# Kernel tuning notes

Measured on AMD Instinct MI355X. Metric: run time of the kernel, lower is better.

The kernel has to match this reference:

```python
import jax, jax.numpy as jnp
import numpy as np

MIN_STD = 0.1
MAX_STD = 1.0
LOG2PI = float(np.log(2.0 * np.pi))


def setup_inputs() -> dict:
    key = jax.random.key(0)
    ks = jax.random.split(key, 5)
    B, D, N, L, H = 512, 256, 32768, 128, 512
    x = jax.random.normal(ks[0], (B, D), dtype=jnp.float32)
    log_w = jax.random.normal(ks[1], (N,), dtype=jnp.float32)
    z = jax.random.normal(ks[2], (N, L), dtype=jnp.float32)
    W1 = jax.random.normal(ks[3], (L, H), dtype=jnp.float32) * (1.0 / np.sqrt(L))
    b1 = jnp.zeros((H,), dtype=jnp.float32)
    W2 = jax.random.normal(ks[4], (H, 2 * D), dtype=jnp.float32) * (1.0 / np.sqrt(H))
    b2 = jnp.zeros((2 * D,), dtype=jnp.float32)
    return {"x": x, "log_w": log_w, "z": z, "W1": W1, "b1": b1, "W2": W2, "b2": b2, "k": 16}


def _get_params(zz, W1, b1, W2, b2):
    # net: 2-layer MLP, then chunk into (mu, logvar); std = clamp(softplus(logvar)+min_std)
    h = jax.nn.relu(zz @ W1 + b1)
    raw = h @ W2 + b2
    mu, logvar = jnp.split(raw, 2, axis=1)
    std = jnp.clip(jax.nn.softplus(logvar) + MIN_STD, MIN_STD, MAX_STD)
    return mu, std


def reference(x, log_w, z, W1, b1, W2, b2, k):
    B, D = x.shape
    # ---- stage 1 (torch.no_grad): full [B, N] Gaussian log-likelihood matrix ----
    mu, std = _get_params(z, W1, b1, W2, b2)          # [N, D]
    inv_var = 1.0 / (std * std)                        # [N, D]
    # sum_d logN(x_d; mu_d, std_d) expanded into matmuls to avoid a [B,N,D] tensor
    lp = (-0.5 * (x * x) @ inv_var.T                   # [B, N]
          + x @ (mu * inv_var).T
          - 0.5 * jnp.sum(mu * mu * inv_var, axis=1)[None, :]
          - jnp.sum(jnp.log(std), axis=1)[None, :]
          - 0.5 * D * LOG2PI)
    scores = lp + log_w[None, :]                       # [B, N]
    _, idx = jax.lax.top_k(scores, k)                  # [B, k]
    z_top = z[idx]                                     # [B, k, L] gather
    # ---- stage 2: recompute NLL only for the top-k components (with grad) ----
    mu2, std2 = _get_params(z_top.reshape(B * k, -1), W1, b1, W2, b2)
    mu2 = mu2.reshape(B, k, D)
    std2 = std2.reshape(B, k, D)
    diff = (x[:, None, :] - mu2) / std2                # [B, k, D]
    lp_topk = jnp.sum(-0.5 * diff * diff - jnp.log(std2), axis=-1) - 0.5 * D * LOG2PI
    return lp_topk                                     # [B, k]
```

## Files before the change

kernel.cpp:

```cpp
#include <hip/hip_runtime.h>
#include <math.h>

#define NCOMP 32768
#define LDIM  128
#define HDIM  512
#define DDIM  256
#define BROWS 512
#define KTOP  16

#define NEG_HALF_D_LOG2PI (-235.24844f)

typedef short bf16x8 __attribute__((ext_vector_type(8)));
typedef float f32x4  __attribute__((ext_vector_type(4)));
typedef unsigned short ushort_t;
typedef unsigned int uint_t;
typedef unsigned long long u64_t;

__device__ __forceinline__ ushort_t f2bf(float f) {
  uint_t u = __float_as_uint(f);
  u = u + 0x7fffu + ((u >> 16) & 1u);
  return (ushort_t)(u >> 16);
}
__device__ __forceinline__ float bf2f(ushort_t h) {
  return __uint_as_float(((uint_t)h) << 16);
}

__device__ __forceinline__ void load_lds16(const ushort_t* g, ushort_t* l) {
  __builtin_amdgcn_global_load_lds(
      (const __attribute__((address_space(1))) unsigned int*)g,
      (__attribute__((address_space(3))) unsigned int*)l, 16, 0, 0);
}

__global__ __launch_bounds__(256) void prep_kernel(
    const float* __restrict__ x, const float* __restrict__ z,
    const float* __restrict__ W1, const float* __restrict__ W2,
    ushort_t* __restrict__ z16, ushort_t* __restrict__ W1t,
    ushort_t* __restrict__ W2t, ushort_t* __restrict__ Xs) {
  const int blk = blockIdx.x, tid = threadIdx.x;
  if (blk < 4096) {
    int i = (blk * 256 + tid) * 4;
    float4 v = *(const float4*)&z[i];
    z16[i + 0] = f2bf(v.x);
    z16[i + 1] = f2bf(v.y);
    z16[i + 2] = f2bf(v.z);
    z16[i + 3] = f2bf(v.w);
  } else if (blk < 4352) {
    int i = (blk - 4096) * 256 + tid;
    int r = i >> 9, c = i & 511;
    W1t[(size_t)c * 128 + r] = f2bf(W1[i]);
  } else if (blk < 5376) {
    int i = (blk - 4352) * 256 + tid;
    int r = i >> 9, c = i & 511;
    W2t[(size_t)c * 512 + r] = f2bf(W2[i]);
  } else {
    int i = (blk - 5376) * 256 + tid;
    int b = i >> 8, d = i & 255;
    float xv = x[i];
    size_t base = (size_t)b * 512;
    Xs[base + d]       = f2bf(xv * xv);
    Xs[base + 256 + d] = f2bf(xv);
  }
}

__global__ __launch_bounds__(256) void params_kernel(const float* __restrict__ raw,
                                                     ushort_t* __restrict__ Ps,
                                                     float* __restrict__ cvec) {
  const int w = threadIdx.x >> 6, lane = threadIdx.x & 63;
  const int n = blockIdx.x * 4 + w;
  size_t rb = (size_t)n * 512;
  float4 mu4 = *(const float4*)(raw + rb + lane * 4);
  float4 lv4 = *(const float4*)(raw + rb + 256 + lane * 4);
  float mus[4] = {mu4.x, mu4.y, mu4.z, mu4.w};
  float lvs[4] = {lv4.x, lv4.y, lv4.z, lv4.w};
  ushort4 o0, o1, o2, o3;
  ushort_t* p0 = &o0.x; ushort_t* p1 = &o1.x;
  ushort_t* p2 = &o2.x; ushort_t* p3 = &o3.x;
  float part = 0.f;
  #pragma unroll
  for (int e = 0; e < 4; e++) {
    float lv = lvs[e];
    float sp = (lv > 20.f) ? lv : log1pf(expf(lv));
    float sd = fminf(sp + 0.1f, 1.0f);
    float iv = 1.0f / (sd * sd);
    float v0 = -0.5f * iv;
    float v1 = mus[e] * iv;
    ushort_t h0 = f2bf(v0), h1 = f2bf(v1);
    p0[e] = h0; p1[e] = h1;
    p2[e] = f2bf(v0 - bf2f(h0));
    p3[e] = f2bf(v1 - bf2f(h1));
    part += -0.5f * mus[e] * mus[e] * iv - logf(sd);
  }
  size_t pb = (size_t)n * 1024;
  *(ushort4*)(Ps + pb + lane * 4)       = o0;
  *(ushort4*)(Ps + pb + 256 + lane * 4) = o1;
  *(ushort4*)(Ps + pb + 512 + lane * 4) = o2;
  *(ushort4*)(Ps + pb + 768 + lane * 4) = o3;
  #pragma unroll
  for (int off = 32; off > 0; off >>= 1) part += __shfl_down(part, off, 64);
  if (lane == 0) cvec[n] = part + NEG_HALF_D_LOG2PI;
}

template<int EPI>
__global__ __launch_bounds__(512, 2) void gemm256(
    const ushort_t* __restrict__ A, int lda,
    const ushort_t* __restrict__ B, int ldb,
    const float* __restrict__ bias,
    void* __restrict__ Cout, int ldc,
    int nsteps, int sps,
    int kbA0, int kbA1, int kbA2,
    int kbB0, int kbB1, int kbB2,
    int nShort, int shortIsM) {
  __shared__ __align__(16) ushort_t As[2][16384];
  __shared__ __align__(16) ushort_t Bs[2][16384];

  const int tid = threadIdx.x;
  const int lane = tid & 63, wid = tid >> 6;
  const int wr = wid >> 2, wc = wid & 3;

  const int cpx = gridDim.x >> 3;
  const int newid = (blockIdx.x & 7) * cpx + (blockIdx.x >> 3);
  const int s = newid % nShort, l = newid / nShort;
  const int m0 = (shortIsM ? s : l) * 256;
  const int n0 = (shortIsM ? l : s) * 256;

  const ushort_t* pA[4];
  const ushort_t* pB[4];
  #pragma unroll
  for (int r = 0; r < 4; r++) {
    int p = r * 512 + tid;
    int row = p >> 3;
    int col = ((p & 7) ^ (row & 7)) * 8;
    pA[r] = A + (size_t)(m0 + row) * lda + col;
    pB[r] = B + (size_t)(n0 + row) * ldb + col;
  }

  int aoff[8], boff[4];
  #pragma unroll
  for (int i = 0; i < 8; i++) {
    int ra = wr * 128 + i * 16 + (lane & 15);
    aoff[i] = (ra * 128 + ((lane >> 4) * 16)) ^ ((ra & 7) << 4);
  }
  #pragma unroll
  for (int j = 0; j < 4; j++) {
    int rb = wc * 64 + j * 16 + (lane & 15);
    boff[j] = (rb * 128 + ((lane >> 4) * 16)) ^ ((rb & 7) << 4);
  }

  f32x4 acc[8][4];
  #pragma unroll
  for (int i = 0; i < 8; i++)
    #pragma unroll
    for (int j = 0; j < 4; j++)
      acc[i][j] = (f32x4){0.f, 0.f, 0.f, 0.f};

  auto stage = [&](int buf, int step) {
    int sg = (step >= sps) ? ((step >= 2 * sps) ? 2 : 1) : 0;
    int ks = (step - sg * sps) << 6;
    int kA = ((sg == 0) ? kbA0 : (sg == 1) ? kbA1 : kbA2) + ks;
    int kB = ((sg == 0) ? kbB0 : (sg == 1) ? kbB1 : kbB2) + ks;
    #pragma unroll
    for (int r = 0; r < 4; r++) {
      load_lds16(pA[r] + kA, &As[buf][(r * 512 + tid) * 8]);
      load_lds16(pB[r] + kB, &Bs[buf][(r * 512 + tid) * 8]);
    }
  };

  stage(0, 0);
  __syncthreads();

  int cur = 0;
  for (int step = 0; step < nsteps; ++step) {
    if (step + 1 < nsteps) stage(cur ^ 1, step + 1);

    const char* Ab = (const char*)As[cur];
    const char* Bb = (const char*)Bs[cur];
    #pragma unroll
    for (int kh = 0; kh < 2; ++kh) {
      bf16x8 af[8], bfr[4];
      #pragma unroll
      for (int i = 0; i < 8; i++) af[i] = *(const bf16x8*)(Ab + (aoff[i] ^ (kh << 6)));
      #pragma unroll
      for (int j = 0; j < 4; j++) bfr[j] = *(const bf16x8*)(Bb + (boff[j] ^ (kh << 6)));
      #pragma unroll
      for (int i = 0; i < 8; i++)
        #pragma unroll
        for (int j = 0; j < 4; j++)
          acc[i][j] = __builtin_amdgcn_mfma_f32_16x16x32_bf16(af[i], bfr[j], acc[i][j], 0, 0, 0);
    }
    __syncthreads();
    cur ^= 1;
  }

  float bv[4];
  #pragma unroll
  for (int j = 0; j < 4; j++)
    bv[j] = bias[n0 + wc * 64 + j * 16 + (lane & 15)];
  #pragma unroll
  for (int i = 0; i < 8; i++) {
    int rowb = m0 + wr * 128 + i * 16 + ((lane >> 4) << 2);
    #pragma unroll
    for (int r = 0; r < 4; r++) {
      #pragma unroll
      for (int j = 0; j < 4; j++) {
        int col = n0 + wc * 64 + j * 16 + (lane & 15);
        float v = acc[i][j][r] + bv[j];
        if (EPI == 0) {
          v = fmaxf(v, 0.f);
          ((ushort_t*)Cout)[(size_t)(rowb + r) * ldc + col] = f2bf(v);
        } else {
          ((float*)Cout)[(size_t)(rowb + r) * ldc + col] = v;
        }
      }
    }
  }
}

__device__ __forceinline__ u64_t shfl_up1_u64(u64_t v) {
  uint_t lo = (uint_t)v, hi = (uint_t)(v >> 32);
  lo = __shfl_up(lo, 1, 64); hi = __shfl_up(hi, 1, 64);
  return ((u64_t)hi << 32) | lo;
}
__device__ __forceinline__ u64_t shfl_u64(u64_t v, int src) {
  uint_t lo = (uint_t)v, hi = (uint_t)(v >> 32);
  lo = __shfl(lo, src, 64); hi = __shfl(hi, src, 64);
  return ((u64_t)hi << 32) | lo;
}
__device__ __forceinline__ void insert_step(u64_t& key, u64_t cand, int lane) {
  u64_t kup = shfl_up1_u64(key);
  if (lane == 0) kup = ~0ULL;
  if (cand > key) key = (cand > kup) ? kup : cand;
}

__global__ __launch_bounds__(256) void topk_kernel(const float* __restrict__ lp,
                                                   const float* __restrict__ log_w,
                                                   float* __restrict__ out) {
  const int b = blockIdx.x;
  const int tid = threadIdx.x;
  const int w = tid >> 6, lane = tid & 63;
  const float* row = lp + (size_t)b * NCOMP;

  u64_t key = 0;
  u64_t theta = 0;

  const int base = w * 8192;
  for (int c = 0; c < 32; ++c) {
    int n0 = base + c * 256 + lane * 4;
    float4 s4 = *(const float4*)&row[n0];
    float4 w4 = *(const float4*)&log_w[n0];
    float ss[4] = {s4.x + w4.x, s4.y + w4.y, s4.z + w4.z, s4.w + w4.w};
    #pragma unroll
    for (int e = 0; e < 4; e++) {
      uint_t u = __float_as_uint(ss[e]);
      u = (u & 0x80000000u) ? ~u : (u | 0x80000000u);
      u64_t k = ((u64_t)u << 32) | (u64_t)(0xFFFFFFFFu - (uint_t)(n0 + e));
      u64_t m = __ballot(k > theta);
      if (m) {
        do {
          int src = __ffsll((long long)m) - 1;
          m &= m - 1;
          u64_t cand = shfl_u64(k, src);
          insert_step(key, cand, lane);
        } while (m);
        theta = shfl_u64(key, 15);
      }
    }
  }

  __shared__ u64_t sk[64];
  if (lane < 16) sk[w * 16 + lane] = key;
  __syncthreads();
  if (w == 0) {
    u64_t th = shfl_u64(key, 15);
    for (int t = 16; t < 64; ++t) {
      u64_t cand = sk[t];
      if (cand > th) {
        insert_step(key, cand, lane);
        th = shfl_u64(key, 15);
      }
    }
    if (lane < 16) {
      uint_t idx = 0xFFFFFFFFu - (uint_t)key;
      out[(size_t)b * KTOP + lane] = row[idx];
    }
  }
}

extern "C" void kernel_launch(void* const* d_in, const int* in_sizes, int n_in,
                              void* d_out, int out_size, void* d_ws, size_t ws_size,
                              hipStream_t stream) {
  const float* x     = (const float*)d_in[0];
  const float* log_w = (const float*)d_in[1];
  const float* z     = (const float*)d_in[2];
  const float* W1    = (const float*)d_in[3];
  const float* b1    = (const float*)d_in[4];
  const float* W2    = (const float*)d_in[5];
  const float* b2    = (const float*)d_in[6];
  float* out = (float*)d_out;

  char* p = (char*)d_ws;
  float* raw   = (float*)p;    p += (size_t)NCOMP * 512 * 4;
  float* cvec  = (float*)p;    p += (size_t)NCOMP * 4;
  ushort_t* Ps = (ushort_t*)p; p += (size_t)NCOMP * 1024 * 2;
  ushort_t* h16= (ushort_t*)p; p += (size_t)NCOMP * 512 * 2;
  ushort_t* z16= (ushort_t*)p; p += (size_t)NCOMP * 128 * 2;
  ushort_t* W1t= (ushort_t*)p; p += (size_t)512 * 128 * 2;
  ushort_t* W2t= (ushort_t*)p; p += (size_t)512 * 512 * 2;
  ushort_t* Xs = (ushort_t*)p; p += (size_t)512 * 512 * 2;
  float* lp = raw;

  hipLaunchKernelGGL(prep_kernel, dim3(5888), dim3(256), 0, stream,
                     x, z, W1, W2, z16, W1t, W2t, Xs);

  hipLaunchKernelGGL((gemm256<0>), dim3(256), dim3(512), 0, stream,
                     z16, LDIM, W1t, LDIM, b1, h16, HDIM,
                     2, 2, 0, 0, 0, 0, 0, 0, 2, 0);
  hipLaunchKernelGGL((gemm256<1>), dim3(256), dim3(512), 0, stream,
                     h16, HDIM, W2t, HDIM, b2, raw, HDIM,
                     8, 8, 0, 0, 0, 0, 0, 0, 2, 0);
  hipLaunchKernelGGL(params_kernel, dim3(NCOMP / 4), dim3(256), 0, stream,
                     raw, Ps, cvec);
  hipLaunchKernelGGL((gemm256<1>), dim3(256), dim3(512), 0, stream,
                     Xs, 512, Ps, 1024, cvec, lp, NCOMP,
                     16, 8, 0, 0, 0, 0, 512, 0, 2, 1);
  hipLaunchKernelGGL(topk_kernel, dim3(BROWS), dim3(256), 0, stream, lp, log_w, out);
}
```

Baseline: 206.0 us.

## Deepen GEMM LDS pipeline to four stages with K=32 tiles and vmcnt waits

Replaces the double-buffered K=64 LDS pipeline with a four-buffer ring of K=32 tiles, issuing loads three stages ahead. Explicit vmcnt waits and a single raw barrier per step replace the full syncthreads. The LDS swizzle is reworked so two rows pack into each 128-byte line. The goal is to hide global-load latency better while keeping the same LDS footprint. In exchange there are more loop iterations, and the hand-placed waitcnt and barrier scheduling must stay correct.

New measurement: 218.2 us. 6.0% more time.

```diff
diff --git a/kernel.cpp b/kernel.cpp
--- a/kernel.cpp
+++ b/kernel.cpp
@@ -30,6 +30,9 @@
       (const __attribute__((address_space(1))) unsigned int*)g,
       (__attribute__((address_space(3))) unsigned int*)l, 16, 0, 0);
 }
+
+#define SBAR() do { __builtin_amdgcn_sched_barrier(0); __builtin_amdgcn_s_barrier(); __builtin_amdgcn_sched_barrier(0); } while (0)
+#define VMCNT(n) asm volatile("s_waitcnt vmcnt(" #n ")" ::: "memory")
 
 __global__ __launch_bounds__(256) void prep_kernel(
     const float* __restrict__ x, const float* __restrict__ z,
@@ -106,12 +109,12 @@
     const ushort_t* __restrict__ B, int ldb,
     const float* __restrict__ bias,
     void* __restrict__ Cout, int ldc,
-    int nsteps, int sps,
+    int nt, int sps,
     int kbA0, int kbA1, int kbA2,
     int kbB0, int kbB1, int kbB2,
     int nShort, int shortIsM) {
-  __shared__ __align__(16) ushort_t As[2][16384];
-  __shared__ __align__(16) ushort_t Bs[2][16384];
+  __shared__ __align__(16) ushort_t As[4][8192];
+  __shared__ __align__(16) ushort_t Bs[4][8192];
 
   const int tid = threadIdx.x;
   const int lane = tid & 63, wid = tid >> 6;
@@ -123,27 +126,33 @@
   const int m0 = (shortIsM ? s : l) * 256;
   const int n0 = (shortIsM ? l : s) * 256;
 
-  const ushort_t* pA[4];
-  const ushort_t* pB[4];
-  #pragma unroll
-  for (int r = 0; r < 4; r++) {
+  const ushort_t* pA[2];
+  const ushort_t* pB[2];
+  #pragma unroll
+  for (int r = 0; r < 2; r++) {
     int p = r * 512 + tid;
-    int row = p >> 3;
-    int col = ((p & 7) ^ (row & 7)) * 8;
-    pA[r] = A + (size_t)(m0 + row) * lda + col;
-    pB[r] = B + (size_t)(n0 + row) * ldb + col;
+    int srow = p >> 3;
+    int cl = (p & 7) ^ (srow & 7);
+    int row = srow * 2 + (cl >> 2);
+    int kcol = (cl & 3) * 8;
+    pA[r] = A + (size_t)(m0 + row) * lda + kcol;
+    pB[r] = B + (size_t)(n0 + row) * ldb + kcol;
   }
 
   int aoff[8], boff[4];
   #pragma unroll
   for (int i = 0; i < 8; i++) {
     int ra = wr * 128 + i * 16 + (lane & 15);
-    aoff[i] = (ra * 128 + ((lane >> 4) * 16)) ^ ((ra & 7) << 4);
+    int sr = ra >> 1;
+    int cl = ((ra & 1) << 2) | (lane >> 4);
+    aoff[i] = sr * 128 + ((cl ^ (sr & 7)) << 4);
   }
   #pragma unroll
   for (int j = 0; j < 4; j++) {
     int rb = wc * 64 + j * 16 + (lane & 15);
-    boff[j] = (rb * 128 + ((lane >> 4) * 16)) ^ ((rb & 7) << 4);
+    int sr = rb >> 1;
+    int cl = ((rb & 1) << 2) | (lane >> 4);
+    boff[j] = sr * 128 + ((cl ^ (sr & 7)) << 4);
   }
 
   f32x4 acc[8][4];
@@ -153,42 +162,43 @@
     for (int j = 0; j < 4; j++)
       acc[i][j] = (f32x4){0.f, 0.f, 0.f, 0.f};
 
-  auto stage = [&](int buf, int step) {
-    int sg = (step >= sps) ? ((step >= 2 * sps) ? 2 : 1) : 0;
-    int ks = (step - sg * sps) << 6;
+  auto stage = [&](int t) {
+    int buf = t & 3;
+    int sg = (t >= sps) ? ((t >= 2 * sps) ? 2 : 1) : 0;
+    int ks = (t - sg * sps) << 5;
     int kA = ((sg == 0) ? kbA0 : (sg == 1) ? kbA1 : kbA2) + ks;
     int kB = ((sg == 0) ? kbB0 : (sg == 1) ? kbB1 : kbB2) + ks;
     #pragma unroll
-    for (int r = 0; r < 4; r++) {
+    for (int r = 0; r < 2; r++) {
       load_lds16(pA[r] + kA, &As[buf][(r * 512 + tid) * 8]);
       load_lds16(pB[r] + kB, &Bs[buf][(r * 512 + tid) * 8]);
     }
   };
 
-  stage(0, 0);
-  __syncthreads();
-
-  int cur = 0;
-  for (int step = 0; step < nsteps; ++step) {
-    if (step + 1 < nsteps) stage(cur ^ 1, step + 1);
-
-    const char* Ab = (const char*)As[cur];
-    const char* Bb = (const char*)Bs[cur];
-    #pragma unroll
-    for (int kh = 0; kh < 2; ++kh) {
-      bf16x8 af[8], bfr[4];
+  stage(0);
+  if (1 < nt) stage(1);
+  if (2 < nt) stage(2);
+
+  for (int t = 0; t < nt; ++t) {
+    if (t + 3 <= nt) { VMCNT(8); }
+    else if (t + 2 == nt) { VMCNT(4); }
+    else { VMCNT(0); }
+    SBAR();
+    if (t + 3 < nt) stage(t + 3);
+    __builtin_amdgcn_sched_barrier(0);
+
+    const char* Ab = (const char*)(&As[0][0]) + (t & 3) * 16384;
+    const char* Bb = (const char*)(&Bs[0][0]) + (t & 3) * 16384;
+    bf16x8 af[8], bfr[4];
+    #pragma unroll
+    for (int i = 0; i < 8; i++) af[i] = *(const bf16x8*)(Ab + aoff[i]);
+    #pragma unroll
+    for (int j = 0; j < 4; j++) bfr[j] = *(const bf16x8*)(Bb + boff[j]);
+    #pragma unroll
+    for (int i = 0; i < 8; i++)
       #pragma unroll
-      for (int i = 0; i < 8; i++) af[i] = *(const bf16x8*)(Ab + (aoff[i] ^ (kh << 6)));
-      #pragma unroll
-      for (int j = 0; j < 4; j++) bfr[j] = *(const bf16x8*)(Bb + (boff[j] ^ (kh << 6)));
-      #pragma unroll
-      for (int i = 0; i < 8; i++)
-        #pragma unroll
-        for (int j = 0; j < 4; j++)
-          acc[i][j] = __builtin_amdgcn_mfma_f32_16x16x32_bf16(af[i], bfr[j], acc[i][j], 0, 0, 0);
-    }
-    __syncthreads();
-    cur ^= 1;
+      for (int j = 0; j < 4; j++)
+        acc[i][j] = __builtin_amdgcn_mfma_f32_16x16x32_bf16(af[i], bfr[j], acc[i][j], 0, 0, 0);
   }
 
   float bv[4];
@@ -313,14 +323,14 @@
 
   hipLaunchKernelGGL((gemm256<0>), dim3(256), dim3(512), 0, stream,
                      z16, LDIM, W1t, LDIM, b1, h16, HDIM,
-                     2, 2, 0, 0, 0, 0, 0, 0, 2, 0);
+                     4, 4, 0, 0, 0, 0, 0, 0, 2, 0);
   hipLaunchKernelGGL((gemm256<1>), dim3(256), dim3(512), 0, stream,
                      h16, HDIM, W2t, HDIM, b2, raw, HDIM,
-                     8, 8, 0, 0, 0, 0, 0, 0, 2, 0);
+                     16, 16, 0, 0, 0, 0, 0, 0, 2, 0);
   hipLaunchKernelGGL(params_kernel, dim3(NCOMP / 4), dim3(256), 0, stream,
                      raw, Ps, cvec);
   hipLaunchKernelGGL((gemm256<1>), dim3(256), dim3(512), 0, stream,
                      Xs, 512, Ps, 1024, cvec, lp, NCOMP,
-                     16, 8, 0, 0, 0, 0, 512, 0, 2, 1);
+                     32, 16, 0, 0, 0, 0, 512, 0, 2, 1);
   hipLaunchKernelGGL(topk_kernel, dim3(BROWS), dim3(256), 0, stream, lp, log_w, out);
 }
```

## Deepen GEMM prefetch with triple-buffered operand and single barrier per step

Applied to the files above, without the earlier changes.

Replaces the GEMM's double-buffered LDS loop with an asymmetric pipeline. The operand chosen by a template flag gets three LDS buffers and is prefetched two k-steps ahead; the other operand keeps two buffers and is prefetched one step ahead. Explicit vmcnt waits and a single scheduler-pinned barrier per iteration replace the trailing __syncthreads, so global-to-LDS latency is hidden better and there is one fewer sync per step. The cost is LDS rising from 128KB to 160KB per block, and correctness now relies on the manual vmcnt counts matching the load issue order.

Result: slower. 214.0 us (+3.9%).

```diff
diff --git a/kernel.cpp b/kernel.cpp
--- a/kernel.cpp
+++ b/kernel.cpp
@@ -30,6 +30,10 @@
       (const __attribute__((address_space(1))) unsigned int*)g,
       (__attribute__((address_space(3))) unsigned int*)l, 16, 0, 0);
 }
+
+#define SBAR() do { __builtin_amdgcn_sched_barrier(0); __builtin_amdgcn_s_barrier(); __builtin_amdgcn_sched_barrier(0); } while (0)
+#define PIN()  __builtin_amdgcn_sched_barrier(0)
+#define VMCNT(n) asm volatile("s_waitcnt vmcnt(" #n ")" ::: "memory")
 
 __global__ __launch_bounds__(256) void prep_kernel(
     const float* __restrict__ x, const float* __restrict__ z,
@@ -100,18 +104,20 @@
   if (lane == 0) cvec[n] = part + NEG_HALF_D_LOG2PI;
 }
 
-template<int EPI>
+template<int EPI, bool ADEEP>
 __global__ __launch_bounds__(512, 2) void gemm256(
     const ushort_t* __restrict__ A, int lda,
     const ushort_t* __restrict__ B, int ldb,
     const float* __restrict__ bias,
     void* __restrict__ Cout, int ldc,
-    int nsteps, int sps,
+    int nt, int sps,
     int kbA0, int kbA1, int kbA2,
     int kbB0, int kbB1, int kbB2,
     int nShort, int shortIsM) {
-  __shared__ __align__(16) ushort_t As[2][16384];
-  __shared__ __align__(16) ushort_t Bs[2][16384];
+  constexpr int NABUF = ADEEP ? 3 : 2;
+  constexpr int NBBUF = ADEEP ? 2 : 3;
+  __shared__ __align__(16) ushort_t As[NABUF][16384];
+  __shared__ __align__(16) ushort_t Bs[NBBUF][16384];
 
   const int tid = threadIdx.x;
   const int lane = tid & 63, wid = tid >> 6;
@@ -153,27 +159,45 @@
     for (int j = 0; j < 4; j++)
       acc[i][j] = (f32x4){0.f, 0.f, 0.f, 0.f};
 
-  auto stage = [&](int buf, int step) {
-    int sg = (step >= sps) ? ((step >= 2 * sps) ? 2 : 1) : 0;
-    int ks = (step - sg * sps) << 6;
-    int kA = ((sg == 0) ? kbA0 : (sg == 1) ? kbA1 : kbA2) + ks;
-    int kB = ((sg == 0) ? kbB0 : (sg == 1) ? kbB1 : kbB2) + ks;
-    #pragma unroll
-    for (int r = 0; r < 4; r++) {
-      load_lds16(pA[r] + kA, &As[buf][(r * 512 + tid) * 8]);
-      load_lds16(pB[r] + kB, &Bs[buf][(r * 512 + tid) * 8]);
-    }
+  auto stageA = [&](int t) {
+    int sg = (t >= sps) ? ((t >= 2 * sps) ? 2 : 1) : 0;
+    int kA = ((sg == 0) ? kbA0 : (sg == 1) ? kbA1 : kbA2) + ((t - sg * sps) << 6);
+    ushort_t* dst = &As[t % NABUF][0];
+    #pragma unroll
+    for (int r = 0; r < 4; r++)
+      load_lds16(pA[r] + kA, dst + (r * 512 + tid) * 8);
   };
-
-  stage(0, 0);
-  __syncthreads();
-
-  int cur = 0;
-  for (int step = 0; step < nsteps; ++step) {
-    if (step + 1 < nsteps) stage(cur ^ 1, step + 1);
-
-    const char* Ab = (const char*)As[cur];
-    const char* Bb = (const char*)Bs[cur];
+  auto stageB = [&](int t) {
+    int sg = (t >= sps) ? ((t >= 2 * sps) ? 2 : 1) : 0;
+    int kB = ((sg == 0) ? kbB0 : (sg == 1) ? kbB1 : kbB2) + ((t - sg * sps) << 6);
+    ushort_t* dst = &Bs[t % NBBUF][0];
+    #pragma unroll
+    for (int r = 0; r < 4; r++)
+      load_lds16(pB[r] + kB, dst + (r * 512 + tid) * 8);
+  };
+
+  if (ADEEP) {
+    stageB(0); PIN(); stageA(0); PIN(); if (1 < nt) stageA(1); PIN();
+  } else {
+    stageA(0); PIN(); stageB(0); PIN(); if (1 < nt) stageB(1); PIN();
+  }
+
+  for (int t = 0; t < nt; ++t) {
+    if (t < nt - 1) { VMCNT(4); } else { VMCNT(0); }
+    SBAR();
+    if (ADEEP) {
+      if (t + 1 < nt) stageB(t + 1);
+      PIN();
+      if (t + 2 < nt) stageA(t + 2);
+    } else {
+      if (t + 1 < nt) stageA(t + 1);
+      PIN();
+      if (t + 2 < nt) stageB(t + 2);
+    }
+    PIN();
+
+    const char* Ab = (const char*)(&As[0][0]) + (t % NABUF) * 32768;
+    const char* Bb = (const char*)(&Bs[0][0]) + (t % NBBUF) * 32768;
     #pragma unroll
     for (int kh = 0; kh < 2; ++kh) {
       bf16x8 af[8], bfr[4];
@@ -187,8 +211,6 @@
         for (int j = 0; j < 4; j++)
           acc[i][j] = __builtin_amdgcn_mfma_f32_16x16x32_bf16(af[i], bfr[j], acc[i][j], 0, 0, 0);
     }
-    __syncthreads();
-    cur ^= 1;
   }
 
   float bv[4];
@@ -311,15 +333,15 @@
   hipLaunchKernelGGL(prep_kernel, dim3(5888), dim3(256), 0, stream,
                      x, z, W1, W2, z16, W1t, W2t, Xs);
 
-  hipLaunchKernelGGL((gemm256<0>), dim3(256), dim3(512), 0, stream,
+  hipLaunchKernelGGL((gemm256<0, true>), dim3(256), dim3(512), 0, stream,
                      z16, LDIM, W1t, LDIM, b1, h16, HDIM,
                      2, 2, 0, 0, 0, 0, 0, 0, 2, 0);
-  hipLaunchKernelGGL((gemm256<1>), dim3(256), dim3(512), 0, stream,
+  hipLaunchKernelGGL((gemm256<1, true>), dim3(256), dim3(512), 0, stream,
                      h16, HDIM, W2t, HDIM, b2, raw, HDIM,
                      8, 8, 0, 0, 0, 0, 0, 0, 2, 0);
   hipLaunchKernelGGL(params_kernel, dim3(NCOMP / 4), dim3(256), 0, stream,
                      raw, Ps, cvec);
-  hipLaunchKernelGGL((gemm256<1>), dim3(256), dim3(512), 0, stream,
+  hipLaunchKernelGGL((gemm256<1, false>), dim3(256), dim3(512), 0, stream,
                      Xs, 512, Ps, 1024, cvec, lp, NCOMP,
                      16, 8, 0, 0, 0, 0, 512, 0, 2, 1);
   hipLaunchKernelGGL(topk_kernel, dim3(BROWS), dim3(256), 0, stream, lp, log_w, out);
```
